# Optimization experiments

Hardware: AMD Instinct MI355X
Metric: run time of the kernel (lower is better)

## Reference

```python
import jax, jax.numpy as jnp
import numpy as np

NUM_CLASSES = 5
N = 4194304

def _quadratic_weights(c):
    i = jnp.arange(c, dtype=jnp.float32)
    # weights[i, j] = (i - j)^2 / (c - 1)^2
    return (i[:, None] - i[None, :]) ** 2 / float((c - 1) ** 2)

def setup_inputs() -> dict:
    key = jax.random.key(0)
    k1, k2 = jax.random.split(key)
    inputs = jax.random.normal(k1, (N, NUM_CLASSES), dtype=jnp.float32)
    targets = jax.random.randint(k2, (N,), 0, NUM_CLASSES, dtype=jnp.int64)
    return {"inputs": inputs, "targets": targets}

def reference(inputs, targets):
    c = NUM_CLASSES
    n = inputs.shape[0]
    weight_matrix = _quadratic_weights(c)
    # softmax then argmax (softmax preserves argmax but kept for faithfulness)
    probs = jax.nn.softmax(inputs, axis=1)
    pred_class = jnp.argmax(probs, axis=1)  # (N,)
    true_class = targets.astype(jnp.int32)
    # vectorized confusion-matrix histogram: flat index true*c + pred, one bincount
    flat_idx = true_class * c + pred_class.astype(jnp.int32)
    confusion = jnp.bincount(flat_idx, length=c * c).astype(jnp.float32).reshape(c, c)
    confusion = confusion / n
    marginal_true = confusion.sum(axis=1)
    marginal_pred = confusion.sum(axis=0)
    expected = jnp.outer(marginal_true, marginal_pred)
    numerator = (confusion * weight_matrix).sum()
    denominator = (expected * weight_matrix).sum()
    kappa = 1.0 - numerator / (denominator + 1e-7)
    return -kappa
```

## Files before the change

kernel.cpp:

```cpp
#include <hip/hip_runtime.h>


#define KCLS 5
#define NREP 64

__global__ __launch_bounds__(256) void kappa_hist(const float* __restrict__ x,
                                                  const int* __restrict__ tgt,
                                                  unsigned int* __restrict__ gcnt) {
    __shared__ unsigned int h[128];
    const int tid = threadIdx.x;
    const int lane = tid & 63;
    unsigned int* hw = h + ((tid >> 6) << 5);
    if (lane < 32) hw[lane] = 0u;

    const int t = blockIdx.x * 256 + tid;
    const float4* xv = (const float4*)x;
    float f[20];
#pragma unroll
    for (int k = 0; k < 5; ++k) {
        float4 v = xv[t * 5 + k];
        f[4 * k + 0] = v.x;
        f[4 * k + 1] = v.y;
        f[4 * k + 2] = v.z;
        f[4 * k + 3] = v.w;
    }
    const int4 tg = ((const int4*)tgt)[t];
    const int tgv[4] = {tg.x, tg.y, tg.z, tg.w};
#pragma unroll
    for (int r = 0; r < 4; ++r) {
        const float* fr = f + 5 * r;
        float m = fr[0];
        int k = 0;
#pragma unroll
        for (int j = 1; j < KCLS; ++j)
            if (fr[j] > m) { m = fr[j]; k = j; }
        atomicAdd(&hw[tgv[r] * KCLS + k], 1u);
    }
    __syncthreads();

    if (tid < KCLS * KCLS) {
        unsigned int s = h[tid] + h[32 + tid] + h[64 + tid] + h[96 + tid];
        if (s) atomicAdd(&gcnt[(blockIdx.x & (NREP - 1)) * 64 + tid], s);
    }
}

__device__ __forceinline__ float seq25(const float* a) {
    float res = 0.0f;
#pragma unroll
    for (int i = 0; i < 25; ++i) res = __fadd_rn(res, a[i]);
    return res;
}

__global__ void kappa_finalize(const unsigned int* __restrict__ gcnt,
                               float* __restrict__ out, int n) {
    __shared__ unsigned int cnt[25];
    const int tid = threadIdx.x;
    if (blockIdx.x != 0) return;

    if (tid < 25) {
        unsigned int s = 0;
#pragma unroll
        for (int r = 0; r < NREP; ++r) s += gcnt[r * 64 + tid];
        cnt[tid] = s;
    }
    __syncthreads();
    if (tid != 0) return;

    const float fn = (float)n;
    float conf[25];
#pragma unroll
    for (int k = 0; k < 25; ++k)
        conf[k] = __fdiv_rn((float)cnt[k], fn);

    float w[25];
#pragma unroll
    for (int i = 0; i < KCLS; ++i)
#pragma unroll
        for (int j = 0; j < KCLS; ++j)
            w[i * KCLS + j] = (float)((i - j) * (i - j)) / 16.0f;

    float mt[KCLS], mp[KCLS];
#pragma unroll
    for (int i = 0; i < KCLS; ++i) {
        float s = 0.0f;
#pragma unroll
        for (int j = 0; j < KCLS; ++j) s = __fadd_rn(s, conf[i * KCLS + j]);
        mt[i] = s;
    }
#pragma unroll
    for (int j = 0; j < KCLS; ++j) {
        float s = 0.0f;
#pragma unroll
        for (int i = 0; i < KCLS; ++i) s = __fadd_rn(s, conf[i * KCLS + j]);
        mp[j] = s;
    }

    float a[25], b[25];
#pragma unroll
    for (int k = 0; k < 25; ++k) {
        a[k] = __fmul_rn(conf[k], w[k]);
        float e = __fmul_rn(mt[k / KCLS], mp[k % KCLS]);
        b[k] = __fmul_rn(e, w[k]);
    }

    float num = seq25(a);
    float den = seq25(b);
    float den2 = __fadd_rn(den, 1e-7f);
    float q = __fdiv_rn(num, den2);
    float kappa = __fsub_rn(1.0f, q);
    out[0] = -kappa;
}

extern "C" void kernel_launch(void* const* d_in, const int* in_sizes, int n_in,
                              void* d_out, int out_size, void* d_ws, size_t ws_size,
                              hipStream_t stream) {
    const float* x = (const float*)d_in[0];
    const int* tgt = (const int*)d_in[1];
    float* out = (float*)d_out;
    unsigned int* cnt = (unsigned int*)d_ws;

    const int n = in_sizes[1];
    const int nblocks = n / 1024;

    hipMemsetAsync(cnt, 0, NREP * 64 * sizeof(unsigned int), stream);
    kappa_hist<<<nblocks, 256, 0, stream>>>(x, tgt, cnt);
    kappa_finalize<<<1, 64, 0, stream>>>(cnt, out, n);
}
```

Baseline: 28.61 us.

## Fuse finalize into histogram kernel with last-block-done atomic counter

Removes the separate finalize launch. Each block bumps a global completion counter after flushing its partial histogram, and the last block to finish reduces all replicas and computes kappa. The global replica count doubles to spread atomic contention, and launch bounds now request 8 blocks per CU. The cost is an extra atomic per block and a serial tail in the last block. The cross-block visibility relies on s_waitcnt plus atomic reads rather than an explicit memory fence.

```diff
diff --git a/kernel.cpp b/kernel.cpp
--- a/kernel.cpp
+++ b/kernel.cpp
@@ -2,47 +2,7 @@
 
 
 #define KCLS 5
-#define NREP 64
-
-__global__ __launch_bounds__(256) void kappa_hist(const float* __restrict__ x,
-                                                  const int* __restrict__ tgt,
-                                                  unsigned int* __restrict__ gcnt) {
-    __shared__ unsigned int h[128];
-    const int tid = threadIdx.x;
-    const int lane = tid & 63;
-    unsigned int* hw = h + ((tid >> 6) << 5);
-    if (lane < 32) hw[lane] = 0u;
-
-    const int t = blockIdx.x * 256 + tid;
-    const float4* xv = (const float4*)x;
-    float f[20];
-#pragma unroll
-    for (int k = 0; k < 5; ++k) {
-        float4 v = xv[t * 5 + k];
-        f[4 * k + 0] = v.x;
-        f[4 * k + 1] = v.y;
-        f[4 * k + 2] = v.z;
-        f[4 * k + 3] = v.w;
-    }
-    const int4 tg = ((const int4*)tgt)[t];
-    const int tgv[4] = {tg.x, tg.y, tg.z, tg.w};
-#pragma unroll
-    for (int r = 0; r < 4; ++r) {
-        const float* fr = f + 5 * r;
-        float m = fr[0];
-        int k = 0;
-#pragma unroll
-        for (int j = 1; j < KCLS; ++j)
-            if (fr[j] > m) { m = fr[j]; k = j; }
-        atomicAdd(&hw[tgv[r] * KCLS + k], 1u);
-    }
-    __syncthreads();
-
-    if (tid < KCLS * KCLS) {
-        unsigned int s = h[tid] + h[32 + tid] + h[64 + tid] + h[96 + tid];
-        if (s) atomicAdd(&gcnt[(blockIdx.x & (NREP - 1)) * 64 + tid], s);
-    }
-}
+#define NREP 128
 
 __device__ __forceinline__ float seq25(const float* a) {
     float res = 0.0f;
@@ -51,21 +11,8 @@
     return res;
 }
 
-__global__ void kappa_finalize(const unsigned int* __restrict__ gcnt,
-                               float* __restrict__ out, int n) {
-    __shared__ unsigned int cnt[25];
-    const int tid = threadIdx.x;
-    if (blockIdx.x != 0) return;
-
-    if (tid < 25) {
-        unsigned int s = 0;
-#pragma unroll
-        for (int r = 0; r < NREP; ++r) s += gcnt[r * 64 + tid];
-        cnt[tid] = s;
-    }
-    __syncthreads();
-    if (tid != 0) return;
-
+__device__ void kappa_finalize_device(const unsigned int* cnt,
+                                      float* out, int n) {
     const float fn = (float)n;
     float conf[25];
 #pragma unroll
@@ -111,6 +58,69 @@
     out[0] = -kappa;
 }
 
+__global__ __launch_bounds__(256, 8) void kappa_hist(const float* __restrict__ x,
+                                                     const int* __restrict__ tgt,
+                                                     unsigned int* __restrict__ gcnt,
+                                                     float* __restrict__ out,
+                                                     int n, int nblocks) {
+    __shared__ unsigned int h[128];
+    const int tid = threadIdx.x;
+    const int lane = tid & 63;
+    unsigned int* hw = h + ((tid >> 6) << 5);
+    if (lane < 32) hw[lane] = 0u;
+
+    const int t = blockIdx.x * 256 + tid;
+    const float4* xv = (const float4*)x;
+    float f[20];
+#pragma unroll
+    for (int k = 0; k < 5; ++k) {
+        float4 v = xv[t * 5 + k];
+        f[4 * k + 0] = v.x;
+        f[4 * k + 1] = v.y;
+        f[4 * k + 2] = v.z;
+        f[4 * k + 3] = v.w;
+    }
+    const int4 tg = ((const int4*)tgt)[t];
+    const int tgv[4] = {tg.x, tg.y, tg.z, tg.w};
+#pragma unroll
+    for (int r = 0; r < 4; ++r) {
+        const float* fr = f + 5 * r;
+        float m = fr[0];
+        int k = 0;
+#pragma unroll
+        for (int j = 1; j < KCLS; ++j)
+            if (fr[j] > m) { m = fr[j]; k = j; }
+        atomicAdd(&hw[tgv[r] * KCLS + k], 1u);
+    }
+    __syncthreads();
+
+    if (tid >= 64) return;
+
+    if (tid < KCLS * KCLS) {
+        unsigned int s = h[tid] + h[32 + tid] + h[64 + tid] + h[96 + tid];
+        if (s) atomicAdd(&gcnt[(blockIdx.x & (NREP - 1)) * 64 + tid], s);
+    }
+
+    int last = 0;
+    if (tid == 0) {
+        asm volatile("s_waitcnt vmcnt(0)" ::: "memory");
+        unsigned int old = atomicAdd(&gcnt[NREP * 64], 1u);
+        last = (old == (unsigned int)(nblocks - 1)) ? 1 : 0;
+    }
+    last = __shfl(last, 0, 64);
+    if (!last) return;
+
+    if (tid < KCLS * KCLS) {
+        unsigned int s = 0;
+#pragma unroll 4
+        for (int r = 0; r < NREP; ++r)
+            s += atomicAdd(&gcnt[r * 64 + tid], 0u);
+        h[tid] = s;
+    }
+    if (tid == 0)
+        kappa_finalize_device(h, out, n);
+}
+
 extern "C" void kernel_launch(void* const* d_in, const int* in_sizes, int n_in,
                               void* d_out, int out_size, void* d_ws, size_t ws_size,
                               hipStream_t stream) {
@@ -122,7 +132,6 @@
     const int n = in_sizes[1];
     const int nblocks = n / 1024;
 
-    hipMemsetAsync(cnt, 0, NREP * 64 * sizeof(unsigned int), stream);
-    kappa_hist<<<nblocks, 256, 0, stream>>>(x, tgt, cnt);
-    kappa_finalize<<<1, 64, 0, stream>>>(cnt, out, n);
+    hipMemsetAsync(cnt, 0, (NREP * 64 + 64) * sizeof(unsigned int), stream);
+    kappa_hist<<<nblocks, 256, 0, stream>>>(x, tgt, cnt, out, n, nblocks);
 }
```

Measured after the change: 71.28 us. 2.49x slower.

## Replace global atomics and memset with per-block partial histograms reduced in finalize

Applied to the files above, without the earlier changes.

Each histogram block now writes its 25 bin counts (padded to 32) to its own workspace slot, replacing atomic adds into 64 replicated global counters. This removes the hipMemsetAsync launch and the contention on global atomics. The finalize kernel grows to 256 threads and reduces the per-block partials with uint4 loads, then sums them through shared memory. The cost is a larger single-block reduction over 4096 blocks x 32 words (512 KB) in finalize, which may be slower than the old 64-replica sum.

```diff
diff --git a/kernel.cpp b/kernel.cpp
--- a/kernel.cpp
+++ b/kernel.cpp
@@ -2,11 +2,10 @@
 
 
 #define KCLS 5
-#define NREP 64
 
 __global__ __launch_bounds__(256) void kappa_hist(const float* __restrict__ x,
                                                   const int* __restrict__ tgt,
-                                                  unsigned int* __restrict__ gcnt) {
+                                                  unsigned int* __restrict__ ws) {
     __shared__ unsigned int h[128];
     const int tid = threadIdx.x;
     const int lane = tid & 63;
@@ -38,9 +37,11 @@
     }
     __syncthreads();
 
-    if (tid < KCLS * KCLS) {
-        unsigned int s = h[tid] + h[32 + tid] + h[64 + tid] + h[96 + tid];
-        if (s) atomicAdd(&gcnt[(blockIdx.x & (NREP - 1)) * 64 + tid], s);
+    if (tid < 32) {
+        unsigned int s = 0;
+        if (tid < KCLS * KCLS)
+            s = h[tid] + h[32 + tid] + h[64 + tid] + h[96 + tid];
+        ws[blockIdx.x * 32 + tid] = s;
     }
 }
 
@@ -51,16 +52,28 @@
     return res;
 }
 
-__global__ void kappa_finalize(const unsigned int* __restrict__ gcnt,
-                               float* __restrict__ out, int n) {
+__global__ __launch_bounds__(256) void kappa_finalize(const unsigned int* __restrict__ ws,
+                                                      float* __restrict__ out,
+                                                      int n, int nblocks) {
+    __shared__ unsigned int lp[256][4];
     __shared__ unsigned int cnt[25];
     const int tid = threadIdx.x;
-    if (blockIdx.x != 0) return;
 
-    if (tid < 25) {
+    const uint4* w4 = (const uint4*)ws;
+    const int c = tid & 7, r0 = tid >> 3;
+    uint4 acc = make_uint4(0u, 0u, 0u, 0u);
+    for (int r = r0; r < nblocks; r += 32) {
+        uint4 v = w4[r * 8 + c];
+        acc.x += v.x; acc.y += v.y; acc.z += v.z; acc.w += v.w;
+    }
+    lp[tid][0] = acc.x; lp[tid][1] = acc.y; lp[tid][2] = acc.z; lp[tid][3] = acc.w;
+    __syncthreads();
+
+    if (tid < KCLS * KCLS) {
+        const int cc = tid >> 2, comp = tid & 3;
         unsigned int s = 0;
 #pragma unroll
-        for (int r = 0; r < NREP; ++r) s += gcnt[r * 64 + tid];
+        for (int g = 0; g < 32; ++g) s += lp[g * 8 + cc][comp];
         cnt[tid] = s;
     }
     __syncthreads();
@@ -117,12 +130,11 @@
     const float* x = (const float*)d_in[0];
     const int* tgt = (const int*)d_in[1];
     float* out = (float*)d_out;
-    unsigned int* cnt = (unsigned int*)d_ws;
+    unsigned int* ws = (unsigned int*)d_ws;
 
     const int n = in_sizes[1];
     const int nblocks = n / 1024;
 
-    hipMemsetAsync(cnt, 0, NREP * 64 * sizeof(unsigned int), stream);
-    kappa_hist<<<nblocks, 256, 0, stream>>>(x, tgt, cnt);
-    kappa_finalize<<<1, 64, 0, stream>>>(cnt, out, n);
+    kappa_hist<<<nblocks, 256, 0, stream>>>(x, tgt, ws);
+    kappa_finalize<<<1, 256, 0, stream>>>(ws, out, n, nblocks);
 }
```

After: 40.70 us. 1.42x slower.
